# Kernel optimization log

Hardware: AMD Instinct MI355X
Metric: run time of the kernel (lower is better)

The kernel has to match this reference:

```python
import jax, jax.numpy as jnp
import numpy as np

B, IN, MEM, CTX, H = 8192, 1024, 1024, 1024, 4
DH = CTX // H

def setup_inputs() -> dict:
    key = jax.random.key(0)
    ks = jax.random.split(key, 20)
    s = 0.02
    d = {
        'input_tensor': jax.random.normal(ks[0], (B, IN), jnp.float32),
        'previous_memory': jax.random.normal(ks[1], (B, MEM), jnp.float32),
        # MultiheadAttention packed in_proj (q,k,v) and out_proj
        'in_proj_w': jax.random.normal(ks[2], (3 * CTX, CTX), jnp.float32) * s,
        'in_proj_b': jnp.zeros((3 * CTX,), jnp.float32),
        'out_proj_w': jax.random.normal(ks[3], (CTX, CTX), jnp.float32) * s,
        'out_proj_b': jnp.zeros((CTX,), jnp.float32),
        # input/memory projections
        'ip_w': jax.random.normal(ks[4], (CTX, IN), jnp.float32) * s,
        'ip_b': jnp.zeros((CTX,), jnp.float32),
        'mp_w': jax.random.normal(ks[5], (CTX, MEM), jnp.float32) * s,
        'mp_b': jnp.zeros((CTX,), jnp.float32),
        # forget / output gates
        'fg_w': jax.random.normal(ks[6], (MEM, MEM + IN), jnp.float32) * s,
        'fg_b': jnp.zeros((MEM,), jnp.float32),
        'og_w': jax.random.normal(ks[7], (MEM, MEM), jnp.float32) * s,
        'og_b': jnp.zeros((MEM,), jnp.float32),
        # GRUCell weights (PyTorch layout: [3*hidden, in], gates order r,z,n)
        'gru_w_ih': jax.random.normal(ks[8], (3 * MEM, CTX), jnp.float32) * s,
        'gru_b_ih': jnp.zeros((3 * MEM,), jnp.float32),
        'gru_w_hh': jax.random.normal(ks[9], (3 * MEM, MEM), jnp.float32) * s,
        'gru_b_hh': jnp.zeros((3 * MEM,), jnp.float32),
    }
    return d

def _forward(input_tensor, previous_memory, in_proj_w, in_proj_b, out_proj_w, out_proj_b,
             ip_w, ip_b, mp_w, mp_b, fg_w, fg_b, og_w, og_b,
             gru_w_ih, gru_b_ih, gru_w_hh, gru_b_hh):
    # projections
    pi = input_tensor @ ip_w.T + ip_b          # [B, CTX] (query; also context/value)
    pm = previous_memory @ mp_w.T + mp_b       # [B, CTX] (key)
    # MHA with q_len = kv_len = 1: softmax over a single key -> weights = 1
    wq, wk, wv = jnp.split(in_proj_w, 3, axis=0)
    bq, bk, bv = jnp.split(in_proj_b, 3, axis=0)
    q = (pi @ wq.T + bq).reshape(B, H, DH)
    k = (pm @ wk.T + bk).reshape(B, H, DH)
    v = (pi @ wv.T + bv).reshape(B, H, DH)
    scores = jnp.sum(q * k, axis=-1, keepdims=True) / jnp.sqrt(jnp.float32(DH))  # [B,H,1]
    w = jax.nn.softmax(scores, axis=-1)        # all ones (single key)
    attn = (w * v).reshape(B, CTX)             # == v
    context_aware = attn @ out_proj_w.T + out_proj_b  # [B, CTX]
    attention_weights = jnp.mean(w, axis=1)[:, None, :]  # [B,1,1], avg over heads
    # forget gate
    forget_in = jnp.concatenate([previous_memory, input_tensor], axis=-1)
    fgate = jax.nn.sigmoid(forget_in @ fg_w.T + fg_b)
    gated_mem = previous_memory * fgate
    # GRUCell (PyTorch semantics)
    gi = context_aware @ gru_w_ih.T + gru_b_ih
    gh = gated_mem @ gru_w_hh.T + gru_b_hh
    gi_r, gi_z, gi_n = jnp.split(gi, 3, axis=-1)
    gh_r, gh_z, gh_n = jnp.split(gh, 3, axis=-1)
    r = jax.nn.sigmoid(gi_r + gh_r)
    z = jax.nn.sigmoid(gi_z + gh_z)
    n = jnp.tanh(gi_n + r * gh_n)
    updated = (1.0 - z) * n + z * gated_mem
    ogate = jax.nn.sigmoid(updated @ og_w.T + og_b)
    return updated * ogate, attention_weights

def reference(input_tensor, previous_memory, in_proj_w, in_proj_b, out_proj_w, out_proj_b,
              ip_w, ip_b, mp_w, mp_b, fg_w, fg_b, og_w, og_b,
              gru_w_ih, gru_b_ih, gru_w_hh, gru_b_hh):
    return _forward(input_tensor, previous_memory, in_proj_w, in_proj_b, out_proj_w, out_proj_b,
                    ip_w, ip_b, mp_w, mp_b, fg_w, fg_b, og_w, og_b,
                    gru_w_ih, gru_b_ih, gru_w_hh, gru_b_hh)
```

## Files before the change

### kernel.cpp

```cpp
#include <hip/hip_runtime.h>
#include <cstdint>
#include <cstddef>


typedef __bf16 bf16;
typedef bf16 bf16x4 __attribute__((ext_vector_type(4)));
typedef bf16 bf16x8 __attribute__((ext_vector_type(8)));
typedef float f32x4 __attribute__((ext_vector_type(4)));

#define B_ROWS 8192

__device__ __forceinline__ float sigmoid_f(float x) {
    return 1.0f / (1.0f + __expf(-x));
}
__device__ __forceinline__ float tanh_f(float x) {
    return 1.0f - 2.0f / (__expf(2.0f * x) + 1.0f);
}

template <int EPI>
__device__ __forceinline__ void g256_core(
    bf16* lds,
    const bf16* A1, int lda1, const bf16* W1, int ldw1, int nt1,
    const bf16* A2, int lda2, const bf16* W2, int ldw2, int nt2,
    const float* bias1, const float* bias2,
    int N, int brow, int bcol,
    bf16* out_bf, float* out_f32,
    const float* aux_f32, const bf16* aux_bf,
    const bf16* grz, const bf16* gni, const bf16* gat)
{
    bf16* sA = lds;
    bf16* sB = lds + 3 * 256 * 32;

    const int tid  = threadIdx.x;
    const int lane = tid & 63;
    const int wave = tid >> 6;
    const int wm   = wave >> 1;
    const int wn   = wave & 1;
    const int lrow = lane & 15;
    const int lq   = lane >> 4;

    f32x4 acc[8][4];
#pragma unroll
    for (int i = 0; i < 8; ++i)
#pragma unroll
        for (int j = 0; j < 4; ++j) {
            f32x4 z = {0.0f, 0.0f, 0.0f, 0.0f};
            acc[i][j] = z;
        }

    auto stage = [&](bf16* dA, bf16* dB, int kt) {
        const bf16* Ab; int lda; const bf16* Wb; int ldw; int k0;
        if (kt < nt1) { Ab = A1; lda = lda1; Wb = W1; ldw = ldw1; k0 = kt << 5; }
        else          { Ab = A2; lda = lda2; Wb = W2; ldw = ldw2; k0 = (kt - nt1) << 5; }
#pragma unroll
        for (int i = 0; i < 4; ++i) {
            const int s   = tid + i * 256;
            const int row = s >> 2;
            const int col = (((s & 3) ^ ((s >> 3) & 3)) << 3);
            const bf16* gp = Ab + (size_t)(brow + row) * lda + (k0 + col);
            __builtin_amdgcn_global_load_lds(
                (const __attribute__((address_space(1))) void*)gp,
                (__attribute__((address_space(3))) void*)(&dA[s * 8]),
                16, 0, 0);
        }
#pragma unroll
        for (int i = 0; i < 2; ++i) {
            const int s   = tid + i * 256;
            const int row = s >> 2;
            const int col = (((s & 3) ^ ((s >> 3) & 3)) << 3);
            const bf16* gp = Wb + (size_t)(bcol + row) * ldw + (k0 + col);
            __builtin_amdgcn_global_load_lds(
                (const __attribute__((address_space(1))) void*)gp,
                (__attribute__((address_space(3))) void*)(&dB[s * 8]),
                16, 0, 0);
        }
    };

    const int NT = nt1 + nt2;

    bf16* a0 = sA;           bf16* b0 = sB;
    bf16* a1 = sA + 8192;    bf16* b1 = sB + 4096;
    bf16* a2 = sA + 16384;   bf16* b2 = sB + 8192;

    stage(a0, b0, 0);
    stage(a1, b1, 1);
    asm volatile("s_waitcnt vmcnt(6)" ::: "memory");
    __builtin_amdgcn_s_barrier();
    __builtin_amdgcn_sched_barrier(0);

    for (int kt = 0; kt < NT; ++kt) {
        bf16x8 av[8], bv[4];
#pragma unroll
        for (int i = 0; i < 8; ++i) {
            const int r = wm * 128 + i * 16 + lrow;
            av[i] = *(const bf16x8*)&a0[r * 32 + ((lq ^ ((r >> 1) & 3)) << 3)];
        }
#pragma unroll
        for (int j = 0; j < 4; ++j) {
            const int r = wn * 64 + j * 16 + lrow;
            bv[j] = *(const bf16x8*)&b0[r * 32 + ((lq ^ ((r >> 1) & 3)) << 3)];
        }

        stage(a2, b2, kt + 2 < NT ? kt + 2 : NT - 1);

#pragma unroll
        for (int i = 0; i < 8; ++i)
#pragma unroll
            for (int j = 0; j < 4; ++j)
                acc[i][j] = __builtin_amdgcn_mfma_f32_16x16x32_bf16(
                    av[i], bv[j], acc[i][j], 0, 0, 0);

        __builtin_amdgcn_sched_barrier(0);
        asm volatile("s_waitcnt vmcnt(6)" ::: "memory");
        __builtin_amdgcn_s_barrier();
        __builtin_amdgcn_sched_barrier(0);

        bf16* ta = a0; a0 = a1; a1 = a2; a2 = ta;
        bf16* tb = b0; b0 = b1; b1 = b2; b2 = tb;
    }

    asm volatile("s_waitcnt vmcnt(0)" ::: "memory");
    __syncthreads();

    if constexpr (EPI == 0) {
        bf16* cb = lds;
#pragma unroll
        for (int j = 0; j < 4; ++j) {
            const int col = wn * 64 + j * 16 + lrow;
            float bj = bias1[bcol + col];
            if (bias2) bj += bias2[bcol + col];
#pragma unroll
            for (int i = 0; i < 8; ++i) {
                const int rowb = wm * 128 + i * 16 + lq * 4;
#pragma unroll
                for (int r = 0; r < 4; ++r)
                    cb[(rowb + r) * 136 + col] = (bf16)(acc[i][j][r] + bj);
            }
        }
        __syncthreads();
#pragma unroll
        for (int p = 0; p < 16; ++p) {
            const int row = p * 16 + (tid >> 4);
            const int col = (tid & 15) * 8;
            bf16x8 v = *(const bf16x8*)&cb[row * 136 + col];
            *(bf16x8*)&out_bf[(size_t)(brow + row) * N + bcol + col] = v;
        }
    } else {
        float* cf = (float*)lds;
#pragma unroll
        for (int h = 0; h < 2; ++h) {
            if (wm == h) {
#pragma unroll
                for (int j = 0; j < 4; ++j) {
                    const int col = wn * 64 + j * 16 + lrow;
                    const float bj = bias1[bcol + col];
#pragma unroll
                    for (int i = 0; i < 8; ++i) {
                        const int rl = i * 16 + lq * 4;
#pragma unroll
                        for (int r = 0; r < 4; ++r)
                            cf[(rl + r) * 132 + col] = acc[i][j][r] + bj;
                    }
                }
            }
            __syncthreads();
#pragma unroll
            for (int p = 0; p < 16; ++p) {
                const int idx = p * 256 + tid;
                const int row = idx >> 5;
                const int ch  = idx & 31;
                f32x4 v = *(const f32x4*)&cf[row * 132 + ch * 4];
                const int grow = brow + h * 128 + row;
                const int gcol = bcol + ch * 4;
                const size_t gidx = (size_t)grow * N + gcol;
                if constexpr (EPI == 1) {
                    f32x4 a4 = *(const f32x4*)&aux_f32[gidx];
                    bf16x4 o;
#pragma unroll
                    for (int e = 0; e < 4; ++e)
                        o[e] = (bf16)(a4[e] * sigmoid_f(v[e]));
                    *(bf16x4*)&out_bf[gidx] = o;
                } else if constexpr (EPI == 2) {
                    bf16x4 ab = *(const bf16x4*)&aux_bf[gidx];
                    f32x4 o;
#pragma unroll
                    for (int e = 0; e < 4; ++e)
                        o[e] = (float)ab[e] * sigmoid_f(v[e]);
                    *(f32x4*)&out_f32[gidx] = o;
                } else {
                    const bf16* pr = grz + (size_t)grow * 2048 + gcol;
                    bf16x4 rr = *(const bf16x4*)pr;
                    bf16x4 zz = *(const bf16x4*)(pr + 1024);
                    bf16x4 g4 = *(const bf16x4*)&gni[gidx];
                    bf16x4 m4 = *(const bf16x4*)&gat[gidx];
                    bf16x4 o;
#pragma unroll
                    for (int e = 0; e < 4; ++e) {
                        const float r = sigmoid_f((float)rr[e]);
                        const float z = sigmoid_f((float)zz[e]);
                        const float n = tanh_f((float)g4[e] + r * v[e]);
                        o[e] = (bf16)((1.0f - z) * n + z * (float)m4[e]);
                    }
                    *(bf16x4*)&out_bf[gidx] = o;
                }
            }
            __syncthreads();
        }
    }
}

__global__ __launch_bounds__(256, 2) void fgg1_k(
    const bf16* __restrict__ cat, const bf16* __restrict__ wfg,
    const float* __restrict__ fg_b, const float* __restrict__ prev,
    bf16* __restrict__ gated,
    const bf16* __restrict__ wcomb_n, const float* __restrict__ bias_n,
    bf16* __restrict__ gni)
{
    __shared__ bf16 lds[36864];
    const int id = blockIdx.x;
    if (id < 256) {
        const int by = id & 31, bx = id >> 5;
        g256_core<1>(lds, cat, 2048, wfg, 2048, 64,
                     nullptr, 0, nullptr, 0, 0,
                     fg_b, nullptr, 1024, by * 256, bx * 128,
                     gated, nullptr, prev, nullptr, nullptr, nullptr, nullptr);
    } else {
        const int id2 = id - 256;
        const int by = id2 & 31, bx = id2 >> 5;
        g256_core<0>(lds, cat + 1024, 2048, wcomb_n, 1024, 32,
                     nullptr, 0, nullptr, 0, 0,
                     bias_n, nullptr, 1024, by * 256, bx * 128,
                     gni, nullptr, nullptr, nullptr, nullptr, nullptr, nullptr);
    }
}

__global__ __launch_bounds__(256, 2) void g2_k(
    const bf16* __restrict__ x, const bf16* __restrict__ wcomb,
    const bf16* __restrict__ gated, const bf16* __restrict__ whh,
    const float* __restrict__ t3b, const float* __restrict__ bhh,
    bf16* __restrict__ grz)
{
    __shared__ bf16 lds[36864];
    const int by = blockIdx.x & 31, bx = blockIdx.x >> 5;
    g256_core<0>(lds, x, 2048, wcomb, 1024, 32,
                 gated, 1024, whh, 1024, 32,
                 t3b, bhh, 2048, by * 256, bx * 128,
                 grz, nullptr, nullptr, nullptr, nullptr, nullptr, nullptr);
}

__global__ __launch_bounds__(256, 2) void g3_k(
    const bf16* __restrict__ gated, const bf16* __restrict__ whh_n,
    const float* __restrict__ bhh_n,
    const bf16* __restrict__ grz, const bf16* __restrict__ gni,
    bf16* __restrict__ upd)
{
    __shared__ bf16 lds[36864];
    const int by = blockIdx.x & 31, bx = blockIdx.x >> 5;
    g256_core<4>(lds, gated, 1024, whh_n, 1024, 32,
                 nullptr, 0, nullptr, 0, 0,
                 bhh_n, nullptr, 1024, by * 256, bx * 128,
                 upd, nullptr, nullptr, nullptr, grz, gni, gated);
}

__global__ __launch_bounds__(256, 2) void og_k(
    const bf16* __restrict__ upd, const bf16* __restrict__ wog,
    const float* __restrict__ og_b, float* __restrict__ out)
{
    __shared__ bf16 lds[36864];
    const int by = blockIdx.x & 31, bx = blockIdx.x >> 5;
    g256_core<2>(lds, upd, 1024, wog, 1024, 32,
                 nullptr, 0, nullptr, 0, 0,
                 og_b, nullptr, 1024, by * 256, bx * 128,
                 nullptr, out, nullptr, upd, nullptr, nullptr, nullptr);
}

template <int BM>
__device__ __forceinline__ void gemm_core_tb(
    bf16* sA, bf16* sB,
    const bf16* __restrict__ A, int lda,
    const bf16* __restrict__ W, int ldw,
    const float* __restrict__ bias,
    int N, int K, int brow, int bcol, int epi,
    bf16* __restrict__ out_bf, int tld)
{
    constexpr int AI = BM / 32;
    const int tid  = threadIdx.x;
    const int lane = tid & 63;
    const int wave = tid >> 6;
    const int wr   = (wave & 1) * (BM / 2);
    const int wc   = (wave >> 1) * 64;
    const int lrow = lane & 15;
    const int lq   = lane >> 4;

    f32x4 acc[AI][4];
#pragma unroll
    for (int i = 0; i < AI; ++i)
#pragma unroll
        for (int j = 0; j < 4; ++j) {
            f32x4 z = {0.0f, 0.0f, 0.0f, 0.0f};
            acc[i][j] = z;
        }

    auto stage = [&](bf16* dA, bf16* dB, int k0) {
#pragma unroll
        for (int i = 0; i < BM / 64; ++i) {
            const int s   = tid + i * 256;
            const int row = s >> 2;
            const int col = (((s & 3) ^ ((s >> 3) & 3)) << 3);
            const bf16* gp = A + (size_t)(brow + row) * lda + (k0 + col);
            __builtin_amdgcn_global_load_lds(
                (const __attribute__((address_space(1))) void*)gp,
                (__attribute__((address_space(3))) void*)(&dA[s * 8]),
                16, 0, 0);
        }
#pragma unroll
        for (int i = 0; i < 2; ++i) {
            const int s   = tid + i * 256;
            const int row = s >> 2;
            const int col = (((s & 3) ^ ((s >> 3) & 3)) << 3);
            const bf16* gp = W + (size_t)(bcol + row) * ldw + (k0 + col);
            __builtin_amdgcn_global_load_lds(
                (const __attribute__((address_space(1))) void*)gp,
                (__attribute__((address_space(3))) void*)(&dB[s * 8]),
                16, 0, 0);
        }
    };

#define WAIT_LPS()                                                   \
    do {                                                             \
        if constexpr (BM == 128)                                     \
            asm volatile("s_waitcnt vmcnt(4)" ::: "memory");         \
        else                                                         \
            asm volatile("s_waitcnt vmcnt(3)" ::: "memory");         \
    } while (0)

    const int NT = K >> 5;

    bf16* a0 = sA;               bf16* b0 = sB;
    bf16* a1 = sA + BM * 32;     bf16* b1 = sB + 4096;
    bf16* a2 = sA + 2 * BM * 32; bf16* b2 = sB + 2 * 4096;

    stage(a0, b0, 0);
    stage(a1, b1, NT > 1 ? 32 : 0);
    WAIT_LPS();
    __builtin_amdgcn_s_barrier();
    __builtin_amdgcn_sched_barrier(0);

    for (int kt = 0; kt < NT; ++kt) {
        bf16x8 av[AI], bv[4];
#pragma unroll
        for (int i = 0; i < AI; ++i) {
            const int r = wr + i * 16 + lrow;
            av[i] = *(const bf16x8*)&a0[r * 32 + ((lq ^ ((r >> 1) & 3)) << 3)];
        }
#pragma unroll
        for (int j = 0; j < 4; ++j) {
            const int r = wc + j * 16 + lrow;
            bv[j] = *(const bf16x8*)&b0[r * 32 + ((lq ^ ((r >> 1) & 3)) << 3)];
        }

        const int kn = (kt + 2 < NT ? kt + 2 : NT - 1) << 5;
        stage(a2, b2, kn);

#pragma unroll
        for (int i = 0; i < AI; ++i)
#pragma unroll
            for (int j = 0; j < 4; ++j)
                acc[i][j] = __builtin_amdgcn_mfma_f32_16x16x32_bf16(
                    av[i], bv[j], acc[i][j], 0, 0, 0);

        __builtin_amdgcn_sched_barrier(0);
        WAIT_LPS();
        __builtin_amdgcn_s_barrier();
        __builtin_amdgcn_sched_barrier(0);

        bf16* ta = a0; a0 = a1; a1 = a2; a2 = ta;
        bf16* tb = b0; b0 = b1; b1 = b2; b2 = tb;
    }

    asm volatile("s_waitcnt vmcnt(0)" ::: "memory");
#undef WAIT_LPS

#pragma unroll
    for (int j = 0; j < 4; ++j) {
        const int gcol = bcol + wc + j * 16 + lrow;
        const float bj = bias ? bias[gcol] : 0.0f;
#pragma unroll
        for (int i = 0; i < AI; ++i) {
            const int growb = brow + wr + i * 16 + lq * 4;
#pragma unroll
            for (int r = 0; r < 4; ++r) {
                const int grow = growb + r;
                const float val = acc[i][j][r] + bj;
                if (epi == 0) {
                    out_bf[(size_t)grow * N + gcol] = (bf16)val;
                } else {
                    out_bf[(size_t)gcol * tld + grow] = (bf16)val;
                }
            }
        }
    }
}

__global__ __launch_bounds__(256, 2) void gemm64_k(
    const bf16* __restrict__ A, int lda, const bf16* __restrict__ W, int ldw,
    const float* __restrict__ bias, int N, int K, int epi,
    bf16* __restrict__ out_bf, int tld, int nby)
{
    __shared__ bf16 sA[3 * 64 * 32];
    __shared__ bf16 sB[3 * 128 * 32];
    const int by = blockIdx.x % nby;
    const int bx = blockIdx.x / nby;
    gemm_core_tb<64>(sA, sB, A, lda, W, ldw, bias, N, K,
                     by * 64, bx * 128, epi, out_bf, tld);
}

__global__ void prep_k(
    const float* __restrict__ prev, const float* __restrict__ input,
    bf16* __restrict__ cat,
    const float* __restrict__ wv, const float* __restrict__ wop,
    const float* __restrict__ wih, const float* __restrict__ wfg,
    const float* __restrict__ wog, const float* __restrict__ whh,
    bf16* __restrict__ dv, bf16* __restrict__ dop, bf16* __restrict__ dih,
    bf16* __restrict__ dfg, bf16* __restrict__ dog, bf16* __restrict__ dhh,
    const float* __restrict__ ipw, bf16* __restrict__ wipt,
    float* __restrict__ ones)
{
    __shared__ float t[32][33];
    const int b = blockIdx.x;
    if (b < 16384) {
        const int i = b * 256 + threadIdx.x;
        const int row = i >> 9;
        const int c4  = i & 511;
        f32x4 v;
        if (c4 < 256)
            v = ((const f32x4*)prev)[(size_t)row * 256 + c4];
        else
            v = ((const f32x4*)input)[(size_t)row * 256 + (c4 - 256)];
        bf16x4 o = {(bf16)v[0], (bf16)v[1], (bf16)v[2], (bf16)v[3]};
        ((bf16x4*)cat)[i] = o;
    } else if (b < 27648) {
        const int c = (b - 16384) * 256 + threadIdx.x;
        const float* s; bf16* d; int o;
        if (c < 262144)        { s = wv;  d = dv;  o = c; }
        else if (c < 524288)   { s = wop; d = dop; o = c - 262144; }
        else if (c < 1310720)  { s = wih; d = dih; o = c - 524288; }
        else if (c < 1835008)  { s = wfg; d = dfg; o = c - 1310720; }
        else if (c < 2097152)  { s = wog; d = dog; o = c - 1835008; }
        else                   { s = whh; d = dhh; o = c - 2097152; }
        f32x4 v = ((const f32x4*)s)[o];
        bf16x4 w = {(bf16)v[0], (bf16)v[1], (bf16)v[2], (bf16)v[3]};
        ((bf16x4*)d)[o] = w;
    } else if (b < 28672) {
        const int b2 = b - 27648;
        const int bx = (b2 & 31) * 32;
        const int by = (b2 >> 5) * 32;
        const int tx = threadIdx.x & 31, ty = threadIdx.x >> 5;
#pragma unroll
        for (int i = 0; i < 32; i += 8)
            t[ty + i][tx] = ipw[(size_t)(by + ty + i) * 1024 + bx + tx];
        __syncthreads();
#pragma unroll
        for (int i = 0; i < 32; i += 8)
            wipt[(size_t)(bx + ty + i) * 1024 + by + tx] = (bf16)t[tx][ty + i];
    } else {
        const int i = (b - 28672) * 256 + threadIdx.x;
        if (i < 2048) {
            f32x4 one = {1.0f, 1.0f, 1.0f, 1.0f};
            ((f32x4*)ones)[i] = one;
        }
    }
}

__global__ void gemv_k(const float* __restrict__ W, const float* __restrict__ x,
                       const float* __restrict__ b, float* __restrict__ y,
                       int K) {
    int n    = blockIdx.x * 4 + (threadIdx.x >> 6);
    int lane = threadIdx.x & 63;
    const float* row = W + (size_t)n * K;
    float s = 0.0f;
    for (int k = lane * 4; k < K; k += 256) {
        f32x4 w = *(const f32x4*)(row + k);
        f32x4 xv = *(const f32x4*)(x + k);
        s += w[0] * xv[0] + w[1] * xv[1] + w[2] * xv[2] + w[3] * xv[3];
    }
#pragma unroll
    for (int off = 32; off; off >>= 1) s += __shfl_down(s, off);
    if (lane == 0) y[n] = s + b[n];
}

extern "C" void kernel_launch(void* const* d_in, const int* in_sizes, int n_in,
                              void* d_out, int out_size, void* d_ws,
                              size_t ws_size, hipStream_t stream) {
    const float* input      = (const float*)d_in[0];
    const float* prev       = (const float*)d_in[1];
    const float* in_proj_w  = (const float*)d_in[2];
    const float* in_proj_b  = (const float*)d_in[3];
    const float* out_proj_w = (const float*)d_in[4];
    const float* out_proj_b = (const float*)d_in[5];
    const float* ip_w       = (const float*)d_in[6];
    const float* ip_b       = (const float*)d_in[7];
    const float* fg_w  = (const float*)d_in[10];
    const float* fg_b  = (const float*)d_in[11];
    const float* og_w  = (const float*)d_in[12];
    const float* og_b  = (const float*)d_in[13];
    const float* gih_w = (const float*)d_in[14];
    const float* gih_b = (const float*)d_in[15];
    const float* ghh_w = (const float*)d_in[16];
    const float* ghh_b = (const float*)d_in[17];
    float* out = (float*)d_out;

    char* ws = (char*)d_ws;
    const size_t MB = 1024 * 1024;
    bf16* CAT   = (bf16*)(ws);
    bf16* WHHB  = (bf16*)(ws + 32 * MB);
    bf16* GRZ   = (bf16*)(ws + 38 * MB);
    bf16* GNI   = (bf16*)(ws + 70 * MB);
    bf16* GATED = (bf16*)(ws + 86 * MB);
    bf16* UPD   = (bf16*)(ws + 102 * MB);
    bf16* WCOMB = (bf16*)(ws + 118 * MB);
    bf16* WOGB  = (bf16*)(ws + 124 * MB);
    bf16* WFGB  = (bf16*)(ws + 126 * MB);
    bf16* WVB   = (bf16*)(ws + 130 * MB);
    bf16* WOPB  = (bf16*)(ws + 132 * MB);
    bf16* WIHB  = (bf16*)(ws + 134 * MB);
    bf16* WIPT  = (bf16*)(ws + 140 * MB);
    bf16* T1T   = (bf16*)(ws + 142 * MB);
    bf16* T2T   = (bf16*)(ws + 144 * MB);
    float* T1B  = (float*)(ws + 146 * MB);
    float* T2B  = (float*)(ws + 146 * MB + 8192);
    float* T3B  = (float*)(ws + 146 * MB + 16384);

    const int M = B_ROWS;
    dim3 blk(256);

    prep_k<<<dim3(28680), blk, 0, stream>>>(
        prev, input, CAT,
        in_proj_w + 2048 * 1024, out_proj_w, gih_w, fg_w, og_w, ghh_w,
        WVB, WOPB, WIHB, WFGB, WOGB, WHHB,
        ip_w, WIPT, out + (size_t)M * 1024);
    gemv_k<<<dim3(256), blk, 0, stream>>>(in_proj_w + 2048 * 1024, ip_b, in_proj_b + 2048, T1B, 1024);
    gemv_k<<<dim3(256), blk, 0, stream>>>(out_proj_w, T1B, out_proj_b, T2B, 1024);
    gemv_k<<<dim3(768), blk, 0, stream>>>(gih_w, T2B, gih_b, T3B, 1024);
    gemm64_k<<<dim3(128), blk, 0, stream>>>(WVB, 1024, WIPT, 1024, nullptr,
        1024, 1024, 3, T1T, 1024, 16);
    gemm64_k<<<dim3(128), blk, 0, stream>>>(WOPB, 1024, T1T, 1024, nullptr,
        1024, 1024, 3, T2T, 1024, 16);
    gemm64_k<<<dim3(384), blk, 0, stream>>>(WIHB, 1024, T2T, 1024, nullptr,
        1024, 1024, 0, WCOMB, 0, 48);
    fgg1_k<<<dim3(512), blk, 0, stream>>>(
        CAT, WFGB, fg_b, prev, GATED,
        WCOMB + (size_t)2048 * 1024, T3B + 2048, GNI);
    g2_k<<<dim3(512), blk, 0, stream>>>(
        CAT + 1024, WCOMB, GATED, WHHB, T3B, ghh_b, GRZ);
    g3_k<<<dim3(256), blk, 0, stream>>>(
        GATED, WHHB + (size_t)2048 * 1024, ghh_b + 2048, GRZ, GNI, UPD);
    og_k<<<dim3(256), blk, 0, stream>>>(UPD, WOGB, og_b, out);
}
```

Measured before the change: 455.2 us.

## Merge independent GEMV, weight-combine and gate GEMM launches into fewer grouped kernels

Independent small launches are packed into shared grids with block-index dispatch. The first bias GEMV moves into prep_k, the second and third GEMVs ride alongside the weight-combining GEMMs, the forget-gate GEMM runs with the first combine, and the GNI GEMM joins the GRU r/z GEMM. This cuts the launch count from eleven to seven and lets small, underfilled grids overlap with larger work. The risk is uneven block durations inside a fused grid and heavier LDS use for GEMV blocks, which could limit occupancy.

```diff
diff --git a/kernel.cpp b/kernel.cpp
--- a/kernel.cpp
+++ b/kernel.cpp
@@ -209,71 +209,6 @@
     }
 }
 
-__global__ __launch_bounds__(256, 2) void fgg1_k(
-    const bf16* __restrict__ cat, const bf16* __restrict__ wfg,
-    const float* __restrict__ fg_b, const float* __restrict__ prev,
-    bf16* __restrict__ gated,
-    const bf16* __restrict__ wcomb_n, const float* __restrict__ bias_n,
-    bf16* __restrict__ gni)
-{
-    __shared__ bf16 lds[36864];
-    const int id = blockIdx.x;
-    if (id < 256) {
-        const int by = id & 31, bx = id >> 5;
-        g256_core<1>(lds, cat, 2048, wfg, 2048, 64,
-                     nullptr, 0, nullptr, 0, 0,
-                     fg_b, nullptr, 1024, by * 256, bx * 128,
-                     gated, nullptr, prev, nullptr, nullptr, nullptr, nullptr);
-    } else {
-        const int id2 = id - 256;
-        const int by = id2 & 31, bx = id2 >> 5;
-        g256_core<0>(lds, cat + 1024, 2048, wcomb_n, 1024, 32,
-                     nullptr, 0, nullptr, 0, 0,
-                     bias_n, nullptr, 1024, by * 256, bx * 128,
-                     gni, nullptr, nullptr, nullptr, nullptr, nullptr, nullptr);
-    }
-}
-
-__global__ __launch_bounds__(256, 2) void g2_k(
-    const bf16* __restrict__ x, const bf16* __restrict__ wcomb,
-    const bf16* __restrict__ gated, const bf16* __restrict__ whh,
-    const float* __restrict__ t3b, const float* __restrict__ bhh,
-    bf16* __restrict__ grz)
-{
-    __shared__ bf16 lds[36864];
-    const int by = blockIdx.x & 31, bx = blockIdx.x >> 5;
-    g256_core<0>(lds, x, 2048, wcomb, 1024, 32,
-                 gated, 1024, whh, 1024, 32,
-                 t3b, bhh, 2048, by * 256, bx * 128,
-                 grz, nullptr, nullptr, nullptr, nullptr, nullptr, nullptr);
-}
-
-__global__ __launch_bounds__(256, 2) void g3_k(
-    const bf16* __restrict__ gated, const bf16* __restrict__ whh_n,
-    const float* __restrict__ bhh_n,
-    const bf16* __restrict__ grz, const bf16* __restrict__ gni,
-    bf16* __restrict__ upd)
-{
-    __shared__ bf16 lds[36864];
-    const int by = blockIdx.x & 31, bx = blockIdx.x >> 5;
-    g256_core<4>(lds, gated, 1024, whh_n, 1024, 32,
-                 nullptr, 0, nullptr, 0, 0,
-                 bhh_n, nullptr, 1024, by * 256, bx * 128,
-                 upd, nullptr, nullptr, nullptr, grz, gni, gated);
-}
-
-__global__ __launch_bounds__(256, 2) void og_k(
-    const bf16* __restrict__ upd, const bf16* __restrict__ wog,
-    const float* __restrict__ og_b, float* __restrict__ out)
-{
-    __shared__ bf16 lds[36864];
-    const int by = blockIdx.x & 31, bx = blockIdx.x >> 5;
-    g256_core<2>(lds, upd, 1024, wog, 1024, 32,
-                 nullptr, 0, nullptr, 0, 0,
-                 og_b, nullptr, 1024, by * 256, bx * 128,
-                 nullptr, out, nullptr, upd, nullptr, nullptr, nullptr);
-}
-
 template <int BM>
 __device__ __forceinline__ void gemm_core_tb(
     bf16* sA, bf16* sB,
@@ -402,17 +337,22 @@
     }
 }
 
-__global__ __launch_bounds__(256, 2) void gemm64_k(
-    const bf16* __restrict__ A, int lda, const bf16* __restrict__ W, int ldw,
-    const float* __restrict__ bias, int N, int K, int epi,
-    bf16* __restrict__ out_bf, int tld, int nby)
-{
-    __shared__ bf16 sA[3 * 64 * 32];
-    __shared__ bf16 sB[3 * 128 * 32];
-    const int by = blockIdx.x % nby;
-    const int bx = blockIdx.x / nby;
-    gemm_core_tb<64>(sA, sB, A, lda, W, ldw, bias, N, K,
-                     by * 64, bx * 128, epi, out_bf, tld);
+__device__ __forceinline__ void gemv_rows(
+    const float* __restrict__ W, const float* __restrict__ x,
+    const float* __restrict__ b, float* __restrict__ y, int nbase)
+{
+    const int n    = nbase + (threadIdx.x >> 6);
+    const int lane = threadIdx.x & 63;
+    const float* row = W + (size_t)n * 1024;
+    float s = 0.0f;
+    for (int k = lane * 4; k < 1024; k += 256) {
+        f32x4 w = *(const f32x4*)(row + k);
+        f32x4 xv = *(const f32x4*)(x + k);
+        s += w[0] * xv[0] + w[1] * xv[1] + w[2] * xv[2] + w[3] * xv[3];
+    }
+#pragma unroll
+    for (int off = 32; off; off >>= 1) s += __shfl_down(s, off);
+    if (lane == 0) y[n] = s + b[n];
 }
 
 __global__ void prep_k(
@@ -424,7 +364,9 @@
     bf16* __restrict__ dv, bf16* __restrict__ dop, bf16* __restrict__ dih,
     bf16* __restrict__ dfg, bf16* __restrict__ dog, bf16* __restrict__ dhh,
     const float* __restrict__ ipw, bf16* __restrict__ wipt,
-    float* __restrict__ ones)
+    float* __restrict__ ones,
+    const float* __restrict__ ip_b, const float* __restrict__ bv,
+    float* __restrict__ t1b)
 {
     __shared__ float t[32][33];
     const int b = blockIdx.x;
@@ -463,30 +405,123 @@
 #pragma unroll
         for (int i = 0; i < 32; i += 8)
             wipt[(size_t)(bx + ty + i) * 1024 + by + tx] = (bf16)t[tx][ty + i];
-    } else {
+    } else if (b < 28680) {
         const int i = (b - 28672) * 256 + threadIdx.x;
         if (i < 2048) {
             f32x4 one = {1.0f, 1.0f, 1.0f, 1.0f};
             ((f32x4*)ones)[i] = one;
         }
-    }
-}
-
-__global__ void gemv_k(const float* __restrict__ W, const float* __restrict__ x,
-                       const float* __restrict__ b, float* __restrict__ y,
-                       int K) {
-    int n    = blockIdx.x * 4 + (threadIdx.x >> 6);
-    int lane = threadIdx.x & 63;
-    const float* row = W + (size_t)n * K;
-    float s = 0.0f;
-    for (int k = lane * 4; k < K; k += 256) {
-        f32x4 w = *(const f32x4*)(row + k);
-        f32x4 xv = *(const f32x4*)(x + k);
-        s += w[0] * xv[0] + w[1] * xv[1] + w[2] * xv[2] + w[3] * xv[3];
-    }
-#pragma unroll
-    for (int off = 32; off; off >>= 1) s += __shfl_down(s, off);
-    if (lane == 0) y[n] = s + b[n];
+    } else {
+        gemv_rows(wv, ip_b, bv, t1b, (b - 28680) * 4);
+    }
+}
+
+__global__ __launch_bounds__(256, 2) void comb1_k(
+    const bf16* __restrict__ wvb, const bf16* __restrict__ wipt,
+    bf16* __restrict__ t1t,
+    const float* __restrict__ wop_f, const float* __restrict__ t1b,
+    const float* __restrict__ bop, float* __restrict__ t2b,
+    const bf16* __restrict__ cat, const bf16* __restrict__ wfgb,
+    const float* __restrict__ fg_b, const float* __restrict__ prev,
+    bf16* __restrict__ gated)
+{
+    __shared__ bf16 lds[36864];
+    const int b = blockIdx.x;
+    if (b < 128) {
+        const int by = b % 16, bx = b / 16;
+        gemm_core_tb<64>(lds, lds + 3 * 64 * 32, wvb, 1024, wipt, 1024,
+                         nullptr, 1024, 1024, by * 64, bx * 128, 3, t1t, 1024);
+    } else if (b < 384) {
+        gemv_rows(wop_f, t1b, bop, t2b, (b - 128) * 4);
+    } else {
+        const int id = b - 384;
+        const int by = id & 31, bx = id >> 5;
+        g256_core<1>(lds, cat, 2048, wfgb, 2048, 64,
+                     nullptr, 0, nullptr, 0, 0,
+                     fg_b, nullptr, 1024, by * 256, bx * 128,
+                     gated, nullptr, prev, nullptr, nullptr, nullptr, nullptr);
+    }
+}
+
+__global__ __launch_bounds__(256, 2) void comb2_k(
+    const bf16* __restrict__ wopb, const bf16* __restrict__ t1t,
+    bf16* __restrict__ t2t,
+    const float* __restrict__ wih_f, const float* __restrict__ t2b,
+    const float* __restrict__ bih, float* __restrict__ t3b)
+{
+    __shared__ bf16 lds[36864];
+    const int b = blockIdx.x;
+    if (b < 128) {
+        const int by = b % 16, bx = b / 16;
+        gemm_core_tb<64>(lds, lds + 3 * 64 * 32, wopb, 1024, t1t, 1024,
+                         nullptr, 1024, 1024, by * 64, bx * 128, 3, t2t, 1024);
+    } else {
+        gemv_rows(wih_f, t2b, bih, t3b, (b - 128) * 4);
+    }
+}
+
+__global__ __launch_bounds__(256, 2) void gemm64_k(
+    const bf16* __restrict__ A, const bf16* __restrict__ W,
+    bf16* __restrict__ out_bf)
+{
+    __shared__ bf16 sA[3 * 64 * 32];
+    __shared__ bf16 sB[3 * 128 * 32];
+    const int by = blockIdx.x % 48;
+    const int bx = blockIdx.x / 48;
+    gemm_core_tb<64>(sA, sB, A, 1024, W, 1024, nullptr,
+                     1024, 1024, by * 64, bx * 128, 0, out_bf, 0);
+}
+
+__global__ __launch_bounds__(256, 2) void big_k(
+    const bf16* __restrict__ x, const bf16* __restrict__ wcomb,
+    const bf16* __restrict__ gated, const bf16* __restrict__ whh,
+    const float* __restrict__ t3b, const float* __restrict__ bhh,
+    bf16* __restrict__ grz,
+    const bf16* __restrict__ wcomb_n, const float* __restrict__ bias_n,
+    bf16* __restrict__ gni)
+{
+    __shared__ bf16 lds[36864];
+    const int b = blockIdx.x;
+    if (b < 512) {
+        const int by = b & 31, bx = b >> 5;
+        g256_core<0>(lds, x, 2048, wcomb, 1024, 32,
+                     gated, 1024, whh, 1024, 32,
+                     t3b, bhh, 2048, by * 256, bx * 128,
+                     grz, nullptr, nullptr, nullptr, nullptr, nullptr, nullptr);
+    } else {
+        const int id = b - 512;
+        const int by = id & 31, bx = id >> 5;
+        g256_core<0>(lds, x, 2048, wcomb_n, 1024, 32,
+                     nullptr, 0, nullptr, 0, 0,
+                     bias_n, nullptr, 1024, by * 256, bx * 128,
+                     gni, nullptr, nullptr, nullptr, nullptr, nullptr, nullptr);
+    }
+}
+
+__global__ __launch_bounds__(256, 2) void g3_k(
+    const bf16* __restrict__ gated, const bf16* __restrict__ whh_n,
+    const float* __restrict__ bhh_n,
+    const bf16* __restrict__ grz, const bf16* __restrict__ gni,
+    bf16* __restrict__ upd)
+{
+    __shared__ bf16 lds[36864];
+    const int by = blockIdx.x & 31, bx = blockIdx.x >> 5;
+    g256_core<4>(lds, gated, 1024, whh_n, 1024, 32,
+                 nullptr, 0, nullptr, 0, 0,
+                 bhh_n, nullptr, 1024, by * 256, bx * 128,
+                 upd, nullptr, nullptr, nullptr, grz, gni, gated);
+}
+
+__global__ __launch_bounds__(256, 2) void og_k(
+    const bf16* __restrict__ upd, const bf16* __restrict__ wog,
+    const float* __restrict__ og_b, float* __restrict__ out)
+{
+    __shared__ bf16 lds[36864];
+    const int by = blockIdx.x & 31, bx = blockIdx.x >> 5;
+    g256_core<2>(lds, upd, 1024, wog, 1024, 32,
+                 nullptr, 0, nullptr, 0, 0,
+                 og_b, nullptr, 1024, by * 256, bx * 128,
+                 nullptr, out, nullptr, upd, nullptr, nullptr, nullptr);
 }
 
 extern "C" void kernel_launch(void* const* d_in, const int* in_sizes, int n_in,
@@ -534,25 +569,23 @@
     const int M = B_ROWS;
     dim3 blk(256);
 
-    prep_k<<<dim3(28680), blk, 0, stream>>>(
+    prep_k<<<dim3(28936), blk, 0, stream>>>(
         prev, input, CAT,
         in_proj_w + 2048 * 1024, out_proj_w, gih_w, fg_w, og_w, ghh_w,
         WVB, WOPB, WIHB, WFGB, WOGB, WHHB,
-        ip_w, WIPT, out + (size_t)M * 1024);
-    gemv_k<<<dim3(256), blk, 0, stream>>>(in_proj_w + 2048 * 1024, ip_b, in_proj_b + 2048, T1B, 1024);
-    gemv_k<<<dim3(256), blk, 0, stream>>>(out_proj_w, T1B, out_proj_b, T2B, 1024);
-    gemv_k<<<dim3(768), blk, 0, stream>>>(gih_w, T2B, gih_b, T3B, 1024);
-    gemm64_k<<<dim3(128), blk, 0, stream>>>(WVB, 1024, WIPT, 1024, nullptr,
-        1024, 1024, 3, T1T, 1024, 16);
-    gemm64_k<<<dim3(128), blk, 0, stream>>>(WOPB, 1024, T1T, 1024, nullptr,
-        1024, 1024, 3, T2T, 1024, 16);
-    gemm64_k<<<dim3(384), blk, 0, stream>>>(WIHB, 1024, T2T, 1024, nullptr,
-        1024, 1024, 0, WCOMB, 0, 48);
-    fgg1_k<<<dim3(512), blk, 0, stream>>>(
-        CAT, WFGB, fg_b, prev, GATED,
+        ip_w, WIPT, out + (size_t)M * 1024,
+        ip_b, in_proj_b + 2048, T1B);
+    comb1_k<<<dim3(640), blk, 0, stream>>>(
+        WVB, WIPT, T1T,
+        out_proj_w, T1B, out_proj_b, T2B,
+        CAT, WFGB, fg_b, prev, GATED);
+    comb2_k<<<dim3(896), blk, 0, stream>>>(
+        WOPB, T1T, T2T,
+        gih_w, T2B, gih_b, T3B);
+    gemm64_k<<<dim3(384), blk, 0, stream>>>(WIHB, T2T, WCOMB);
+    big_k<<<dim3(768), blk, 0, stream>>>(
+        CAT + 1024, WCOMB, GATED, WHHB, T3B, ghh_b, GRZ,
         WCOMB + (size_t)2048 * 1024, T3B + 2048, GNI);
-    g2_k<<<dim3(512), blk, 0, stream>>>(
-        CAT + 1024, WCOMB, GATED, WHHB, T3B, ghh_b, GRZ);
     g3_k<<<dim3(256), blk, 0, stream>>>(
         GATED, WHHB + (size_t)2048 * 1024, ghh_b + 2048, GRZ, GNI, UPD);
     og_k<<<dim3(256), blk, 0, stream>>>(UPD, WOGB, og_b, out);
```

After: 434.6 us. -4.5%, faster.
